# Performance work log

Measured on AMD Instinct MI355X. Metric: run time of the kernel, lower is better.

Reference implementation:

```python
import jax, jax.numpy as jnp
import numpy as np

HIDDEN = 3072
N_HEADS = 24
N_KV = 8
HEAD_DIM = HIDDEN // N_HEADS          # 128
ROT = int(HEAD_DIM * 0.75)            # 96 (partial rotary)
OP_SIZE = N_HEADS * HEAD_DIM + 2 * N_KV * HEAD_DIM  # 5120
LORA_R = 256
LORA_SCALE = 512.0 / LORA_R           # 2.0
ROPE_THETA = 10000.0
SCALE = HEAD_DIM ** -0.5


def setup_inputs() -> dict:
    key = jax.random.key(0)
    ks = jax.random.split(key, 8)
    B, S = 2, 2048
    hidden_states = jax.random.normal(ks[0], (B, S, HIDDEN), dtype=jnp.float32)
    position_ids = jnp.arange(B * S, dtype=jnp.int64 if jax.config.jax_enable_x64 else jnp.int32).reshape(B, S)
    w = lambda k, o, i: jax.random.normal(k, (o, i), dtype=jnp.float32) * (i ** -0.5)
    return {
        "hidden_states": hidden_states,
        "Wqkv": w(ks[1], OP_SIZE, HIDDEN),
        "Aqkv": w(ks[2], LORA_R, HIDDEN),
        "Bqkv": w(ks[3], OP_SIZE, LORA_R) * 0.01,
        "Wo": w(ks[4], HIDDEN, N_HEADS * HEAD_DIM),
        "Ao": w(ks[5], LORA_R, N_HEADS * HEAD_DIM),
        "Bo": w(ks[6], HIDDEN, LORA_R) * 0.01,
        "position_ids": position_ids,
    }


def _lora_linear(x, W, A, Bm):
    # base GEMM + low-rank LoRA update, scaling = alpha/r
    return x @ W.T + (x @ A.T) @ Bm.T * LORA_SCALE


def _rotate_half(x):
    h = x.shape[-1] // 2
    return jnp.concatenate((-x[..., h:], x[..., :h]), axis=-1)


def reference(hidden_states, Wqkv, Aqkv, Bqkv, Wo, Ao, Bo, position_ids):
    B, S, _ = hidden_states.shape
    qkv = _lora_linear(hidden_states, Wqkv, Aqkv, Bqkv)  # [B,S,5120]
    q_pos = N_HEADS * HEAD_DIM
    kv_pos = N_KV * HEAD_DIM
    q = qkv[..., :q_pos].reshape(B, S, N_HEADS, HEAD_DIM)
    k = qkv[..., q_pos:q_pos + kv_pos].reshape(B, S, N_KV, HEAD_DIM)
    v = qkv[..., q_pos + kv_pos:].reshape(B, S, N_KV, HEAD_DIM)

    # partial RoPE: cos/sin cache over rotary_ndims=96
    inv_freq = 1.0 / (ROPE_THETA ** (jnp.arange(0, ROT, 2, dtype=jnp.float32) / ROT))  # [48]
    freqs = position_ids.astype(jnp.float32)[..., None] * inv_freq  # [B,S,48]
    emb = jnp.concatenate((freqs, freqs), axis=-1)                   # [B,S,96]
    cos = jnp.cos(emb)[:, :, None, :]  # broadcast over head axis (bsnd)
    sin = jnp.sin(emb)[:, :, None, :]

    def rope(x):
        xr, xp = x[..., :ROT], x[..., ROT:]
        xr = xr * cos + _rotate_half(xr) * sin
        return jnp.concatenate((xr, xp), axis=-1)

    q = rope(q)
    k = rope(k)

    # GQA: repeat kv heads to match query heads
    groups = N_HEADS // N_KV
    k = jnp.repeat(k, groups, axis=2)
    v = jnp.repeat(v, groups, axis=2)

    scores = jnp.einsum('bqhd,bkhd->bhqk', q, k) * SCALE  # [B,H,S,S]
    causal = jnp.tril(jnp.ones((S, S), dtype=bool))
    scores = jnp.where(causal, scores, jnp.finfo(scores.dtype).min)
    probs = jax.nn.softmax(scores, axis=-1)
    attn = jnp.einsum('bhqk,bkhd->bqhd', probs, v).reshape(B, S, N_HEADS * HEAD_DIM)
    return _lora_linear(attn, Wo, Ao, Bo)
```

## Files before the change

### kernel.cpp

```cpp
#include <hip/hip_runtime.h>

typedef unsigned short u16;
typedef unsigned int   u32;

typedef __bf16 bf16_t;
typedef bf16_t bf16x8 __attribute__((ext_vector_type(8)));
typedef float  f32x4  __attribute__((ext_vector_type(4)));
typedef u16    u16x8  __attribute__((ext_vector_type(8)));

__device__ __forceinline__ float bf2f(u16 u) { return __uint_as_float(((u32)u) << 16); }
__device__ __forceinline__ u16 f2bf(float f) {
  u32 u = __float_as_uint(f);
  u32 r = u + 0x7fffu + ((u >> 16) & 1u);
  return (u16)(r >> 16);
}
__device__ __forceinline__ float fast_exp2(float x) { return __builtin_amdgcn_exp2f(x); }

__device__ __forceinline__ void gload_lds16(const u16* g, u16* l) {
  __builtin_amdgcn_global_load_lds(
      (const __attribute__((address_space(1))) void*)g,
      (__attribute__((address_space(3))) void*)l,
      16, 0, 0);
}

#define SBAR0() __builtin_amdgcn_sched_barrier(0)
#define HWBAR() __builtin_amdgcn_s_barrier()

__global__ void k_cast_str(const float* __restrict__ in, u16* __restrict__ out,
                           int C8, int L, int off, float scale) {
  const int r  = blockIdx.y;
  const int c8 = blockIdx.x * 128 + threadIdx.x;
  if (c8 >= C8) return;
  const f32x4* p = (const f32x4*)(in + (size_t)r * (C8 * 8) + c8 * 8);
  f32x4 a = p[0], b = p[1];
  u16x8 o;
  o[0] = f2bf(a[0] * scale); o[1] = f2bf(a[1] * scale);
  o[2] = f2bf(a[2] * scale); o[3] = f2bf(a[3] * scale);
  o[4] = f2bf(b[0] * scale); o[5] = f2bf(b[1] * scale);
  o[6] = f2bf(b[2] * scale); o[7] = f2bf(b[3] * scale);
  *(u16x8*)(out + (size_t)r * L + off + c8 * 8) = o;
}

__global__ void k_red4_cast(const float* __restrict__ t4, u16* __restrict__ out,
                            int C8, int L, int off, float scale, size_t plane) {
  const int r  = blockIdx.y;
  const int c8 = blockIdx.x * 64 + threadIdx.x;
  if (c8 >= C8) return;
  size_t base = (size_t)r * (C8 * 8) + c8 * 8;
  float s[8];
#pragma unroll
  for (int j = 0; j < 8; ++j) s[j] = 0.f;
#pragma unroll
  for (int p = 0; p < 4; ++p) {
    const f32x4* q = (const f32x4*)(t4 + p * plane + base);
    f32x4 a = q[0], b = q[1];
    s[0] += a[0]; s[1] += a[1]; s[2] += a[2]; s[3] += a[3];
    s[4] += b[0]; s[5] += b[1]; s[6] += b[2]; s[7] += b[3];
  }
  u16x8 o;
#pragma unroll
  for (int j = 0; j < 8; ++j) o[j] = f2bf(s[j] * scale);
  *(u16x8*)(out + (size_t)r * L + off + c8 * 8) = o;
}

__global__ __launch_bounds__(256) void k_gemm_bt_sk(
    const u16* __restrict__ A, const u16* __restrict__ B, float* __restrict__ C,
    int M, int N, int lda, int ldb, int kc) {
  __shared__ u16 As[64][64 + 8];
  __shared__ u16 Bs[64][64 + 8];
  const int tid   = threadIdx.x;
  const int lane  = tid & 63;
  const int w     = tid >> 6;
  const int wm    = (w >> 1) * 32;
  const int wn    = (w & 1) * 32;
  const int row16 = lane & 15;
  const int quad  = lane >> 4;
  const int m0 = blockIdx.y * 64;
  const int n0 = blockIdx.x * 64;
  const int ldr = tid >> 2;
  const int ldc = (tid & 3) * 16;
  const int z   = blockIdx.z;
  float* Cz = C + (size_t)z * M * N;
  const int kbeg = z * kc, kend = kbeg + kc;

  f32x4 acc[2][2] = {};

  for (int k0 = kbeg; k0 < kend; k0 += 64) {
    const u16* ga = A + (size_t)(m0 + ldr) * lda + (k0 + ldc);
    const u16* gb = B + (size_t)(n0 + ldr) * ldb + (k0 + ldc);
    u16x8 a0 = *(const u16x8*)ga;
    u16x8 a1 = *(const u16x8*)(ga + 8);
    u16x8 b0 = *(const u16x8*)gb;
    u16x8 b1 = *(const u16x8*)(gb + 8);
    __syncthreads();
    *(u16x8*)&As[ldr][ldc]     = a0;
    *(u16x8*)&As[ldr][ldc + 8] = a1;
    *(u16x8*)&Bs[ldr][ldc]     = b0;
    *(u16x8*)&Bs[ldr][ldc + 8] = b1;
    __syncthreads();
#pragma unroll
    for (int kk = 0; kk < 64; kk += 32) {
      bf16x8 af0 = *(const bf16x8*)&As[wm + row16][kk + quad * 8];
      bf16x8 af1 = *(const bf16x8*)&As[wm + 16 + row16][kk + quad * 8];
      bf16x8 bg0 = *(const bf16x8*)&Bs[wn + row16][kk + quad * 8];
      bf16x8 bg1 = *(const bf16x8*)&Bs[wn + 16 + row16][kk + quad * 8];
      acc[0][0] = __builtin_amdgcn_mfma_f32_16x16x32_bf16(af0, bg0, acc[0][0], 0, 0, 0);
      acc[0][1] = __builtin_amdgcn_mfma_f32_16x16x32_bf16(af0, bg1, acc[0][1], 0, 0, 0);
      acc[1][0] = __builtin_amdgcn_mfma_f32_16x16x32_bf16(af1, bg0, acc[1][0], 0, 0, 0);
      acc[1][1] = __builtin_amdgcn_mfma_f32_16x16x32_bf16(af1, bg1, acc[1][1], 0, 0, 0);
    }
  }
#pragma unroll
  for (int tm = 0; tm < 2; ++tm)
#pragma unroll
    for (int tn = 0; tn < 2; ++tn) {
      int gm = m0 + wm + tm * 16 + quad * 4;
      int gn = n0 + wn + tn * 16 + row16;
#pragma unroll
      for (int r = 0; r < 4; ++r)
        Cz[(size_t)(gm + r) * N + gn] = acc[tm][tn][r];
    }
}

__device__ __forceinline__ void stage_half(
    int H, int nt4,
    const u16* __restrict__ A, const u16* __restrict__ B, int K,
    int m0, int n0, u16* AsB, u16* BsB,
    int w, int rowin, int colsw) {
  if (H >= nt4) return;
  const int t = H >> 2, slot = H & 3;
  const int half = slot & 1;
  const u16* G = (slot < 2) ? A : B;
  const int r0 = (slot < 2) ? m0 : n0;
  u16* lds = ((slot < 2) ? AsB : BsB) + (t & 1) * 16384 + half * 8192;
  const int k0 = t * 64;
#pragma unroll
  for (int i = 0; i < 2; ++i) {
    const int chunk = w * 2 + i;
    const int row = half * 128 + chunk * 8 + rowin;
    gload_lds16(G + (size_t)(r0 + row) * K + k0 + colsw, lds + chunk * 512);
  }
}

__device__ __forceinline__ bf16x8 frag_ld(const u16* base, int row, int c16) {
  return *(const bf16x8*)(base + row * 64 + ((c16 ^ (row & 7)) << 3));
}

template <int RB>
__device__ __forceinline__ void gemm256_group(
    int k, int nt,
    const u16* __restrict__ A, const u16* __restrict__ B, int K,
    int m0, int n0, u16* AsB, u16* BsB,
    int wr, int wc, int row16, int quad, int w, int rowin, int colsw,
    f32x4 (&acc)[8][4]) {
  const u16* Ab = AsB + RB * 16384;
  const u16* Bb = BsB + RB * 16384;
  const int nt4 = nt * 4;
  bf16x8 a0[4][2], a1[4][2], b0[2][2], b1[2][2];

#pragma unroll
  for (int mf = 0; mf < 4; ++mf)
#pragma unroll
    for (int kk = 0; kk < 2; ++kk)
      a0[mf][kk] = frag_ld(Ab, wr * 128 + mf * 16 + row16, kk * 4 + quad);
#pragma unroll
  for (int nf = 0; nf < 2; ++nf)
#pragma unroll
    for (int kk = 0; kk < 2; ++kk)
      b0[nf][kk] = frag_ld(Bb, wc * 64 + nf * 16 + row16, kk * 4 + quad);
  stage_half(4 * k + 5, nt4, A, B, K, m0, n0, AsB, BsB, w, rowin, colsw);
  SBAR0(); HWBAR(); SBAR0();
  __builtin_amdgcn_s_setprio(1);
#pragma unroll
  for (int mf = 0; mf < 4; ++mf)
#pragma unroll
    for (int nf = 0; nf < 2; ++nf)
#pragma unroll
      for (int kk = 0; kk < 2; ++kk)
        acc[mf][nf] = __builtin_amdgcn_mfma_f32_16x16x32_bf16(a0[mf][kk], b0[nf][kk], acc[mf][nf], 0, 0, 0);
  __builtin_amdgcn_s_setprio(0);
  SBAR0(); HWBAR(); SBAR0();

#pragma unroll
  for (int nf = 0; nf < 2; ++nf)
#pragma unroll
    for (int kk = 0; kk < 2; ++kk)
      b1[nf][kk] = frag_ld(Bb, wc * 64 + 32 + nf * 16 + row16, kk * 4 + quad);
  stage_half(4 * k + 6, nt4, A, B, K, m0, n0, AsB, BsB, w, rowin, colsw);
  SBAR0(); HWBAR(); SBAR0();
  __builtin_amdgcn_s_setprio(1);
#pragma unroll
  for (int mf = 0; mf < 4; ++mf)
#pragma unroll
    for (int nf = 0; nf < 2; ++nf)
#pragma unroll
      for (int kk = 0; kk < 2; ++kk)
        acc[mf][2 + nf] = __builtin_amdgcn_mfma_f32_16x16x32_bf16(a0[mf][kk], b1[nf][kk], acc[mf][2 + nf], 0, 0, 0);
  __builtin_amdgcn_s_setprio(0);
  SBAR0(); HWBAR(); SBAR0();

#pragma unroll
  for (int mf = 0; mf < 4; ++mf)
#pragma unroll
    for (int kk = 0; kk < 2; ++kk)
      a1[mf][kk] = frag_ld(Ab, wr * 128 + 64 + mf * 16 + row16, kk * 4 + quad);
  stage_half(4 * k + 7, nt4, A, B, K, m0, n0, AsB, BsB, w, rowin, colsw);
  SBAR0(); HWBAR(); SBAR0();
  __builtin_amdgcn_s_setprio(1);
#pragma unroll
  for (int mf = 0; mf < 4; ++mf)
#pragma unroll
    for (int nf = 0; nf < 2; ++nf)
#pragma unroll
      for (int kk = 0; kk < 2; ++kk)
        acc[4 + mf][nf] = __builtin_amdgcn_mfma_f32_16x16x32_bf16(a1[mf][kk], b0[nf][kk], acc[4 + mf][nf], 0, 0, 0);
  __builtin_amdgcn_s_setprio(0);
  SBAR0(); HWBAR(); SBAR0();

  stage_half(4 * k + 8, nt4, A, B, K, m0, n0, AsB, BsB, w, rowin, colsw);
  SBAR0();
  if (k < nt - 2) { asm volatile("s_waitcnt vmcnt(2)" ::: "memory"); }
  else            { asm volatile("s_waitcnt vmcnt(0)" ::: "memory"); }
  HWBAR(); SBAR0();
  __builtin_amdgcn_s_setprio(1);
#pragma unroll
  for (int mf = 0; mf < 4; ++mf)
#pragma unroll
    for (int nf = 0; nf < 2; ++nf)
#pragma unroll
      for (int kk = 0; kk < 2; ++kk)
        acc[4 + mf][2 + nf] = __builtin_amdgcn_mfma_f32_16x16x32_bf16(a1[mf][kk], b1[nf][kk], acc[4 + mf][2 + nf], 0, 0, 0);
  __builtin_amdgcn_s_setprio(0);
  SBAR0(); HWBAR(); SBAR0();
}

__global__ __launch_bounds__(512, 2) void k_gemm256(
    const u16* __restrict__ A, const u16* __restrict__ B, float* __restrict__ C,
    int M, int N, int K) {
  __shared__ u16 As[2 * 16384];
  __shared__ u16 Bs[2 * 16384];

  const int tid   = threadIdx.x;
  const int lane  = tid & 63;
  const int w     = tid >> 6;
  const int wr    = w >> 2;
  const int wc    = w & 3;
  const int row16 = lane & 15;
  const int quad  = lane >> 4;
  const int rowin = lane >> 3;
  const int colsw = ((lane & 7) ^ (lane >> 3)) << 3;

  const int nwg = (int)gridDim.x;
  const int bid = (int)blockIdx.x;
  const int xcd = bid & 7, rest = bid >> 3;
  const int qq = nwg >> 3, rr = nwg & 7;
  const int wg = (xcd < rr ? xcd * (qq + 1) : rr * (qq + 1) + (xcd - rr) * qq) + rest;
  const int nbx = N >> 8;
  const int m0 = (wg / nbx) << 8;
  const int n0 = (wg % nbx) << 8;

  const int nt = K >> 6;
  f32x4 acc[8][4] = {};

#pragma unroll
  for (int H = 0; H < 5; ++H)
    stage_half(H, nt * 4, A, B, K, m0, n0, As, Bs, w, rowin, colsw);
  asm volatile("s_waitcnt vmcnt(2)" ::: "memory");
  HWBAR(); SBAR0();

  int k = 0;
  for (; k + 1 < nt; k += 2) {
    gemm256_group<0>(k,     nt, A, B, K, m0, n0, As, Bs, wr, wc, row16, quad, w, rowin, colsw, acc);
    gemm256_group<1>(k + 1, nt, A, B, K, m0, n0, As, Bs, wr, wc, row16, quad, w, rowin, colsw, acc);
  }
  if (k < nt)
    gemm256_group<0>(k, nt, A, B, K, m0, n0, As, Bs, wr, wc, row16, quad, w, rowin, colsw, acc);

#pragma unroll
  for (int mi = 0; mi < 8; ++mi) {
    const int gm = m0 + wr * 128 + mi * 16 + quad * 4;
#pragma unroll
    for (int nj = 0; nj < 4; ++nj) {
      const int gn = n0 + wc * 64 + nj * 16 + row16;
#pragma unroll
      for (int r = 0; r < 4; ++r)
        C[(size_t)(gm + r) * N + gn] = acc[mi][nj][r];
    }
  }
}

__global__ void k_rope_tab(const int* __restrict__ pos_ids, float* __restrict__ tab) {
  const int t = threadIdx.x;
  const int r = blockIdx.x * 4 + t / 48;
  const int j = t % 48;
  const float pos = (float)pos_ids[r];
  float invf = powf(10000.0f, -(float)j * (1.0f / 48.0f));
  float e = pos * invf;
  tab[(size_t)r * 96 + j]      = cosf(e);
  tab[(size_t)r * 96 + 48 + j] = sinf(e);
}

__global__ void k_rope_split(const float* __restrict__ qkv, const float* __restrict__ tab,
                             u16* __restrict__ qb, u16* __restrict__ kb) {
  const int r  = blockIdx.x;
  const int hh = blockIdx.y;
  const int d  = threadIdx.x;
  const float* src;
  if (hh < 24) src = qkv + (size_t)r * 5120 + hh * 128;
  else         src = qkv + (size_t)r * 5120 + 3072 + (hh - 24) * 128;
  float x = src[d];
  float outv;
  if (d >= 96) {
    outv = x;
  } else {
    int j = (d < 48) ? d : d - 48;
    float c  = tab[(size_t)r * 96 + j];
    float sn = tab[(size_t)r * 96 + 48 + j];
    if (d < 48) outv = x * c - src[d + 48] * sn;
    else        outv = x * c + src[d - 48] * sn;
  }
  u16 o = f2bf(outv);
  if (hh < 24) qb[((size_t)r * 24 + hh) * 128 + d] = o;
  else         kb[((size_t)r * 8 + (hh - 24)) * 128 + d] = o;
}

__global__ void k_vtrans(const float* __restrict__ qkv, u16* __restrict__ vtg) {
  const int d  = threadIdx.x;
  const int kg = blockIdx.x;
  const int bk = blockIdx.y;
  const int b = bk >> 3, kvh = bk & 7;
  const float* src = qkv + (size_t)(b * 2048 + kg * 8) * 5120 + 4096 + kvh * 128 + d;
  u16x8 pack;
#pragma unroll
  for (int t = 0; t < 8; ++t) pack[t] = f2bf(src[(size_t)t * 5120]);
  *(u16x8*)(vtg + ((size_t)bk * 128 + d) * 2048 + kg * 8) = pack;
}

__global__ __launch_bounds__(512) void k_attn_mfma(
    const u16* __restrict__ qb, const u16* __restrict__ kb, const u16* __restrict__ vtg,
    u16* __restrict__ attnw) {
  __shared__ u16 Ks[64 * 128];
  __shared__ u16 Vt[128 * 64];
  __shared__ u16 Ps[128 * 64];

  const int tid   = threadIdx.x;
  const int lane  = tid & 63;
  const int w     = tid >> 6;
  const int row16 = lane & 15;
  const int quad  = lane >> 4;
  const int qt  = (int)gridDim.x - 1 - (int)blockIdx.x;
  const int bh  = blockIdx.y;
  const int b   = bh / 24;
  const int h   = bh % 24;
  const int kvh = h / 3;
  const int q0  = qt * 128;
  const int qrow = q0 + w * 16 + row16;

  const u16* qbase = qb + (((size_t)(b * 2048 + qrow)) * 24 + h) * 128;
  bf16x8 qfrag[4];
#pragma unroll
  for (int kk = 0; kk < 4; ++kk) qfrag[kk] = *(const bf16x8*)(qbase + kk * 32 + quad * 8);

  const u16* kbbase = kb + ((size_t)(b * 2048) * 8 + kvh) * 128;
  const u16* vtbase = vtg + (size_t)(b * 8 + kvh) * 128 * 2048;

  f32x4 o[8] = {};
  float m_st = -INFINITY;
  float l_st = 0.f;
  const float C1 = 0.08838834764831845f * 1.4426950408889634f;

  const int ntile = 2 * qt + 2;

  u16x8 kr[2], vr[2];
#pragma unroll
  for (int i = 0; i < 2; ++i) {
    int c = tid + i * 512;
    kr[i] = *(const u16x8*)(kbbase + (size_t)(c >> 4) * 1024 + (c & 15) * 8);
  }
#pragma unroll
  for (int i = 0; i < 2; ++i) {
    int c = tid + i * 512;
    vr[i] = *(const u16x8*)(vtbase + (size_t)(c >> 3) * 2048 + (c & 7) * 8);
  }

  for (int t = 0; t < ntile; ++t) {
    const int kb0 = t * 64;
    __syncthreads();
#pragma unroll
    for (int i = 0; i < 2; ++i) {
      int c = tid + i * 512;
      int kk = c >> 4;
      int slot = (c & 15) ^ (kk & 7);
      *(u16x8*)&Ks[kk * 128 + slot * 8] = kr[i];
    }
#pragma unroll
    for (int i = 0; i < 2; ++i) {
      int c = tid + i * 512;
      int d = c >> 3;
      int slot = (c & 7) ^ (d & 7);
      *(u16x8*)&Vt[d * 64 + slot * 8] = vr[i];
    }
    __syncthreads();
    if (t + 1 < ntile) {
      const int nb0 = kb0 + 64;
#pragma unroll
      for (int i = 0; i < 2; ++i) {
        int c = tid + i * 512;
        kr[i] = *(const u16x8*)(kbbase + (size_t)(nb0 + (c >> 4)) * 1024 + (c & 15) * 8);
      }
#pragma unroll
      for (int i = 0; i < 2; ++i) {
        int c = tid + i * 512;
        vr[i] = *(const u16x8*)(vtbase + (size_t)(c >> 3) * 2048 + nb0 + (c & 7) * 8);
      }
    }

    f32x4 s[4] = {};
    __builtin_amdgcn_s_setprio(1);
#pragma unroll
    for (int kk = 0; kk < 4; ++kk) {
#pragma unroll
      for (int nt = 0; nt < 4; ++nt) {
        int krow = nt * 16 + row16;
        bf16x8 kfr = *(const bf16x8*)&Ks[krow * 128 + (((kk * 4 + quad) ^ (krow & 7)) << 3)];
        s[nt] = __builtin_amdgcn_mfma_f32_16x16x32_bf16(kfr, qfrag[kk], s[nt], 0, 0, 0);
      }
    }
    __builtin_amdgcn_s_setprio(0);

    if (t >= 2 * qt) {
#pragma unroll
      for (int nt = 0; nt < 4; ++nt) {
        int kbase = kb0 + nt * 16 + quad * 4;
#pragma unroll
        for (int r = 0; r < 4; ++r)
          if (kbase + r > qrow) s[nt][r] = -INFINITY;
      }
    }

    float mx = s[0][0];
#pragma unroll
    for (int nt = 0; nt < 4; ++nt)
#pragma unroll
      for (int r = 0; r < 4; ++r) mx = fmaxf(mx, s[nt][r]);
    mx = fmaxf(mx, __shfl_xor(mx, 16));
    mx = fmaxf(mx, __shfl_xor(mx, 32));
    float mnew = fmaxf(m_st, mx);
    float alpha = fast_exp2((m_st - mnew) * C1);
    m_st = mnew;
    float rs = 0.f;
#pragma unroll
    for (int nt = 0; nt < 4; ++nt)
#pragma unroll
      for (int r = 0; r < 4; ++r) {
        float p = fast_exp2((s[nt][r] - mnew) * C1);
        s[nt][r] = p;
        rs += p;
      }
    rs += __shfl_xor(rs, 16);
    rs += __shfl_xor(rs, 32);
    l_st = l_st * alpha + rs;
#pragma unroll
    for (int r = 0; r < 4; ++r) {
      float ar = __shfl(alpha, quad * 4 + r, 64);
#pragma unroll
      for (int dt = 0; dt < 8; ++dt) o[dt][r] *= ar;
    }

#pragma unroll
    for (int nt = 0; nt < 4; ++nt)
#pragma unroll
      for (int r = 0; r < 4; ++r) {
        int col = nt * 16 + quad * 4 + r;
        int slot = (col >> 3) ^ (row16 & 7);
        Ps[(w * 16 + row16) * 64 + slot * 8 + (col & 7)] = f2bf(s[nt][r]);
      }

    __builtin_amdgcn_s_setprio(1);
#pragma unroll
    for (int kk2 = 0; kk2 < 2; ++kk2) {
      bf16x8 pa = *(const bf16x8*)&Ps[(w * 16 + row16) * 64 + (((kk2 * 4 + quad) ^ (row16 & 7)) << 3)];
#pragma unroll
      for (int dt = 0; dt < 8; ++dt) {
        int vrow = dt * 16 + row16;
        bf16x8 vfr = *(const bf16x8*)&Vt[vrow * 64 + (((kk2 * 4 + quad) ^ (vrow & 7)) << 3)];
        o[dt] = __builtin_amdgcn_mfma_f32_16x16x32_bf16(pa, vfr, o[dt], 0, 0, 0);
      }
    }
    __builtin_amdgcn_s_setprio(0);
  }

#pragma unroll
  for (int r = 0; r < 4; ++r) {
    float lq = __shfl(l_st, quad * 4 + r, 64);
    float inv = 1.0f / lq;
    int row = q0 + w * 16 + quad * 4 + r;
    size_t obase = ((size_t)(b * 2048 + row)) * 3328 + (size_t)h * 128;
#pragma unroll
    for (int dt = 0; dt < 8; ++dt)
      attnw[obase + dt * 16 + row16] = f2bf(o[dt][r] * inv);
  }
}

#define OFF_XW    ((size_t)0)
#define OFF_WWQ   ((size_t)27262976)
#define OFF_AQKVB ((size_t)61341696)
#define OFF_WWO   ((size_t)62914560)
#define OFF_AOB   ((size_t)83361792)
#define OFF_QKV   ((size_t)84934656)
#define OFF_TA    ((size_t)168820736)
#define OFF_TA4   OFF_QKV
#define OFF_QB    OFF_XW
#define OFF_KB    OFF_WWQ
#define OFF_VTG   (OFF_WWQ + (size_t)8388608)
#define OFF_RTAB  (OFF_WWQ + (size_t)16777216)
#define OFF_ATTNW OFF_QKV
#define OFF_TO4   (OFF_QKV + (size_t)27262976)

extern "C" void kernel_launch(void* const* d_in, const int* in_sizes, int n_in,
                              void* d_out, int out_size, void* d_ws, size_t ws_size,
                              hipStream_t stream) {
  const float* x    = (const float*)d_in[0];
  const float* Wqkv = (const float*)d_in[1];
  const float* Aqkv = (const float*)d_in[2];
  const float* Bqkv = (const float*)d_in[3];
  const float* Wo   = (const float*)d_in[4];
  const float* Ao   = (const float*)d_in[5];
  const float* Bo   = (const float*)d_in[6];
  const int*   pos  = (const int*)d_in[7];
  float* out = (float*)d_out;
  char* ws = (char*)d_ws;

  u16* xw    = (u16*)(ws + OFF_XW);
  u16* wwq   = (u16*)(ws + OFF_WWQ);
  u16* aqkvb = (u16*)(ws + OFF_AQKVB);
  u16* wwo   = (u16*)(ws + OFF_WWO);
  u16* aob   = (u16*)(ws + OFF_AOB);
  float* qkv = (float*)(ws + OFF_QKV);
  float* tA  = (float*)(ws + OFF_TA);
  (void)tA;
  float* tA4 = (float*)(ws + OFF_TA4);
  u16* qb    = (u16*)(ws + OFF_QB);
  u16* kb    = (u16*)(ws + OFF_KB);
  u16* vtg   = (u16*)(ws + OFF_VTG);
  float* rtab = (float*)(ws + OFF_RTAB);
  u16* attnw = (u16*)(ws + OFF_ATTNW);
  float* tO4 = (float*)(ws + OFF_TO4);

  k_cast_str<<<dim3(3, 4096), 128, 0, stream>>>(x,    xw,  384, 3328, 0,    1.f);
  k_cast_str<<<dim3(3, 5120), 128, 0, stream>>>(Wqkv, wwq, 384, 3328, 0,    1.f);
  k_cast_str<<<dim3(1, 5120), 128, 0, stream>>>(Bqkv, wwq,  32, 3328, 3072, 1.f);
  k_cast_str<<<dim3(3, 256),  128, 0, stream>>>(Aqkv, aqkvb, 384, 3072, 0,  1.f);
  k_cast_str<<<dim3(3, 3072), 128, 0, stream>>>(Wo,   wwo, 384, 3328, 0,    1.f);
  k_cast_str<<<dim3(1, 3072), 128, 0, stream>>>(Bo,   wwo,  32, 3328, 3072, 1.f);
  k_cast_str<<<dim3(3, 256),  128, 0, stream>>>(Ao,   aob, 384, 3072, 0,    1.f);

  k_gemm_bt_sk<<<dim3(4, 64, 4), 256, 0, stream>>>(xw, aqkvb, tA4, 4096, 256, 3328, 3072, 768);
  k_red4_cast<<<dim3(1, 4096), 64, 0, stream>>>(tA4, xw, 32, 3328, 3072, 2.f, (size_t)4096 * 256);

  k_gemm256<<<dim3((5120 / 256) * (4096 / 256)), 512, 0, stream>>>(xw, wwq, qkv, 4096, 5120, 3328);

  k_rope_tab<<<dim3(1024), 192, 0, stream>>>(pos, rtab);
  k_rope_split<<<dim3(4096, 32), 128, 0, stream>>>(qkv, rtab, qb, kb);
  k_vtrans<<<dim3(256, 16), 128, 0, stream>>>(qkv, vtg);

  k_attn_mfma<<<dim3(16, 48), 512, 0, stream>>>(qb, kb, vtg, attnw);

  k_gemm_bt_sk<<<dim3(4, 64, 4), 256, 0, stream>>>(attnw, aob, tO4, 4096, 256, 3328, 3072, 768);
  k_red4_cast<<<dim3(1, 4096), 64, 0, stream>>>(tO4, attnw, 32, 3328, 3072, 2.f, (size_t)4096 * 256);

  k_gemm256<<<dim3((3072 / 256) * (4096 / 256)), 512, 0, stream>>>(attnw, wwo, out, 4096, 3072, 3328);
}
```

Before: 736.3 us.

## Restructure attention kernel with 32x32 MFMA, direct-to-LDS double buffering, and register P

Rewrites the flash-attention kernel to use 4 waves of 32 query rows with 32x32x16 MFMAs instead of 8 waves of 16 rows with 16x16x32. K/V tiles are loaded directly into double-buffered LDS via global_load_lds, which overlaps the next tile's load with compute and drops one barrier per tile. P is kept in registers using packed bf16 conversion and lane shuffles instead of a round trip through LDS. It also adds a lazy rescale that skips updating the running max and the O rescale when the max grows only a little, and stages the output through LDS for vectorized stores. The costs are higher register pressure and the extra bounded-error logic in the softmax.

```diff
diff --git a/kernel.cpp b/kernel.cpp
--- a/kernel.cpp
+++ b/kernel.cpp
@@ -6,7 +6,9 @@
 typedef __bf16 bf16_t;
 typedef bf16_t bf16x8 __attribute__((ext_vector_type(8)));
 typedef float  f32x4  __attribute__((ext_vector_type(4)));
+typedef float  f32x16 __attribute__((ext_vector_type(16)));
 typedef u16    u16x8  __attribute__((ext_vector_type(8)));
+typedef u32    u32x4  __attribute__((ext_vector_type(4)));
 
 __device__ __forceinline__ float bf2f(u16 u) { return __uint_as_float(((u32)u) << 16); }
 __device__ __forceinline__ u16 f2bf(float f) {
@@ -336,169 +338,180 @@
   *(u16x8*)(vtg + ((size_t)bk * 128 + d) * 2048 + kg * 8) = pack;
 }
 
-__global__ __launch_bounds__(512) void k_attn_mfma(
+__global__ __launch_bounds__(256) void k_attn_mfma(
     const u16* __restrict__ qb, const u16* __restrict__ kb, const u16* __restrict__ vtg,
     u16* __restrict__ attnw) {
-  __shared__ u16 Ks[64 * 128];
-  __shared__ u16 Vt[128 * 64];
-  __shared__ u16 Ps[128 * 64];
-
-  const int tid   = threadIdx.x;
-  const int lane  = tid & 63;
-  const int w     = tid >> 6;
-  const int row16 = lane & 15;
-  const int quad  = lane >> 4;
-  const int qt  = (int)gridDim.x - 1 - (int)blockIdx.x;
-  const int bh  = blockIdx.y;
-  const int b   = bh / 24;
-  const int h   = bh % 24;
-  const int kvh = h / 3;
-  const int q0  = qt * 128;
-  const int qrow = q0 + w * 16 + row16;
-
-  const u16* qbase = qb + (((size_t)(b * 2048 + qrow)) * 24 + h) * 128;
-  bf16x8 qfrag[4];
-#pragma unroll
-  for (int kk = 0; kk < 4; ++kk) qfrag[kk] = *(const bf16x8*)(qbase + kk * 32 + quad * 8);
+  __shared__ u16 KsA[8192], VtA[8192], KsB[8192], VtB[8192];
+
+  const int tid  = threadIdx.x;
+  const int lane = tid & 63;
+  const int w    = tid >> 6;
+  const int l31  = lane & 31;
+  const int hi   = lane >> 5;
+  const int r7   = lane & 7;
+  const int qt   = (int)gridDim.x - 1 - (int)blockIdx.x;
+  const int bh   = blockIdx.y;
+  const int b    = bh / 24;
+  const int h    = bh % 24;
+  const int kvh  = h / 3;
+  const int q0   = qt * 128;
+  const int qrow = q0 + w * 32 + l31;
+
+  const u16* qrb = qb + (((size_t)(b * 2048 + qrow)) * 24 + h) * 128;
+  bf16x8 qf[8];
+#pragma unroll
+  for (int kk = 0; kk < 8; ++kk) qf[kk] = *(const bf16x8*)(qrb + kk * 16 + hi * 8);
 
   const u16* kbbase = kb + ((size_t)(b * 2048) * 8 + kvh) * 128;
   const u16* vtbase = vtg + (size_t)(b * 8 + kvh) * 128 * 2048;
 
-  f32x4 o[8] = {};
-  float m_st = -INFINITY;
-  float l_st = 0.f;
+  f32x16 o32[4] = {};
+  float m_st = -INFINITY, l_st = 0.f;
   const float C1 = 0.08838834764831845f * 1.4426950408889634f;
-
   const int ntile = 2 * qt + 2;
 
-  u16x8 kr[2], vr[2];
-#pragma unroll
-  for (int i = 0; i < 2; ++i) {
-    int c = tid + i * 512;
-    kr[i] = *(const u16x8*)(kbbase + (size_t)(c >> 4) * 1024 + (c & 15) * 8);
-  }
-#pragma unroll
-  for (int i = 0; i < 2; ++i) {
-    int c = tid + i * 512;
-    vr[i] = *(const u16x8*)(vtbase + (size_t)(c >> 3) * 2048 + (c & 7) * 8);
-  }
+#define STAGE(Kd, Vd, KB0)                                                          \
+  {                                                                                 \
+    _Pragma("unroll")                                                               \
+    for (int i = 0; i < 4; ++i) {                                                   \
+      const int c = w * 4 + i;                                                      \
+      const int rowk = 4 * c + (lane >> 4);                                         \
+      gload_lds16(kbbase + (size_t)((KB0) + rowk) * 1024 +                          \
+                      (((lane & 15) ^ (rowk & 7)) << 3),                            \
+                  (Kd) + c * 512);                                                  \
+      const int rowv = 8 * c + (lane >> 3);                                         \
+      gload_lds16(vtbase + (size_t)rowv * 2048 + (KB0) +                            \
+                      (((lane & 7) ^ (rowv & 7)) << 3),                             \
+                  (Vd) + c * 512);                                                  \
+    }                                                                               \
+  }
+
+  STAGE(KsA, VtA, 0);
+  __syncthreads();
 
   for (int t = 0; t < ntile; ++t) {
     const int kb0 = t * 64;
+    const u16* Kc = (t & 1) ? KsB : KsA;
+    const u16* Vc = (t & 1) ? VtB : VtA;
+    if (t + 1 < ntile) {
+      u16* Kn = (t & 1) ? KsA : KsB;
+      u16* Vn = (t & 1) ? VtA : VtB;
+      STAGE(Kn, Vn, kb0 + 64);
+    }
+
+    f32x16 s[2] = {};
+    __builtin_amdgcn_s_setprio(1);
+#pragma unroll
+    for (int kk = 0; kk < 8; ++kk) {
+#pragma unroll
+      for (int kt = 0; kt < 2; ++kt) {
+        const int row = kt * 32 + l31;
+        bf16x8 kf = *(const bf16x8*)&Kc[row * 128 + (((2 * kk + hi) ^ r7) << 3)];
+        s[kt] = __builtin_amdgcn_mfma_f32_32x32x16_bf16(kf, qf[kk], s[kt], 0, 0, 0);
+      }
+    }
+    __builtin_amdgcn_s_setprio(0);
+
+    if (kb0 >= q0) {
+#pragma unroll
+      for (int kt = 0; kt < 2; ++kt)
+#pragma unroll
+        for (int r = 0; r < 16; ++r) {
+          const int key = kb0 + 32 * kt + (r & 3) + 8 * (r >> 2) + 4 * hi;
+          if (key > qrow) s[kt][r] = -INFINITY;
+        }
+    }
+
+    float tm[16];
+#pragma unroll
+    for (int r = 0; r < 16; ++r) tm[r] = fmaxf(s[0][r], s[1][r]);
+#pragma unroll
+    for (int st = 8; st >= 1; st >>= 1)
+#pragma unroll
+      for (int r = 0; r < 8; ++r)
+        if (r < st) tm[r] = fmaxf(tm[r], tm[r + st]);
+    float mx = fmaxf(tm[0], __shfl_xor(tm[0], 32));
+
+    const bool skip = __all((mx - m_st) * C1 <= 8.0f);
+    if (!skip) {
+      const float mnew = fmaxf(m_st, mx);
+      const float alpha = fast_exp2((m_st - mnew) * C1);
+      l_st *= alpha;
+#pragma unroll
+      for (int dt = 0; dt < 4; ++dt)
+#pragma unroll
+        for (int r = 0; r < 16; ++r) o32[dt][r] *= alpha;
+      m_st = mnew;
+    }
+    const float mc = m_st * C1;
+    float ts[16];
+#pragma unroll
+    for (int r = 0; r < 16; ++r) {
+      float p0 = fast_exp2(__builtin_fmaf(s[0][r], C1, -mc));
+      float p1 = fast_exp2(__builtin_fmaf(s[1][r], C1, -mc));
+      s[0][r] = p0; s[1][r] = p1;
+      ts[r] = p0 + p1;
+    }
+#pragma unroll
+    for (int st = 8; st >= 1; st >>= 1)
+#pragma unroll
+      for (int r = 0; r < 8; ++r)
+        if (r < st) ts[r] += ts[r + st];
+    l_st += ts[0] + __shfl_xor(ts[0], 32);
+
+    bf16x8 pb[4];
+#pragma unroll
+    for (int kt = 0; kt < 2; ++kt) {
+      u32 pk[8];
+#pragma unroll
+      for (int i = 0; i < 8; ++i)
+        asm("v_cvt_pk_bf16_f32 %0, %1, %2"
+            : "=v"(pk[i]) : "v"(s[kt][2 * i]), "v"(s[kt][2 * i + 1]));
+      u32 e0 = __shfl_xor(hi ? pk[0] : pk[2], 32);
+      u32 e1 = __shfl_xor(hi ? pk[1] : pk[3], 32);
+      u32 e2 = __shfl_xor(hi ? pk[4] : pk[6], 32);
+      u32 e3 = __shfl_xor(hi ? pk[5] : pk[7], 32);
+      u32x4 w0, w1;
+      w0[0] = hi ? e0 : pk[0]; w0[1] = hi ? e1 : pk[1];
+      w0[2] = hi ? pk[2] : e0; w0[3] = hi ? pk[3] : e1;
+      w1[0] = hi ? e2 : pk[4]; w1[1] = hi ? e3 : pk[5];
+      w1[2] = hi ? pk[6] : e2; w1[3] = hi ? pk[7] : e3;
+      pb[2 * kt]     = __builtin_bit_cast(bf16x8, w0);
+      pb[2 * kt + 1] = __builtin_bit_cast(bf16x8, w1);
+    }
+
+    __builtin_amdgcn_s_setprio(1);
+#pragma unroll
+    for (int ks = 0; ks < 4; ++ks) {
+#pragma unroll
+      for (int dt = 0; dt < 4; ++dt) {
+        const int vrow = dt * 32 + l31;
+        bf16x8 vf = *(const bf16x8*)&Vc[vrow * 64 + (((2 * ks + hi) ^ r7) << 3)];
+        o32[dt] = __builtin_amdgcn_mfma_f32_32x32x16_bf16(vf, pb[ks], o32[dt], 0, 0, 0);
+      }
+    }
+    __builtin_amdgcn_s_setprio(0);
+
     __syncthreads();
-#pragma unroll
-    for (int i = 0; i < 2; ++i) {
-      int c = tid + i * 512;
-      int kk = c >> 4;
-      int slot = (c & 15) ^ (kk & 7);
-      *(u16x8*)&Ks[kk * 128 + slot * 8] = kr[i];
-    }
-#pragma unroll
-    for (int i = 0; i < 2; ++i) {
-      int c = tid + i * 512;
-      int d = c >> 3;
-      int slot = (c & 7) ^ (d & 7);
-      *(u16x8*)&Vt[d * 64 + slot * 8] = vr[i];
-    }
-    __syncthreads();
-    if (t + 1 < ntile) {
-      const int nb0 = kb0 + 64;
-#pragma unroll
-      for (int i = 0; i < 2; ++i) {
-        int c = tid + i * 512;
-        kr[i] = *(const u16x8*)(kbbase + (size_t)(nb0 + (c >> 4)) * 1024 + (c & 15) * 8);
-      }
-#pragma unroll
-      for (int i = 0; i < 2; ++i) {
-        int c = tid + i * 512;
-        vr[i] = *(const u16x8*)(vtbase + (size_t)(c >> 3) * 2048 + nb0 + (c & 7) * 8);
-      }
-    }
-
-    f32x4 s[4] = {};
-    __builtin_amdgcn_s_setprio(1);
-#pragma unroll
-    for (int kk = 0; kk < 4; ++kk) {
-#pragma unroll
-      for (int nt = 0; nt < 4; ++nt) {
-        int krow = nt * 16 + row16;
-        bf16x8 kfr = *(const bf16x8*)&Ks[krow * 128 + (((kk * 4 + quad) ^ (krow & 7)) << 3)];
-        s[nt] = __builtin_amdgcn_mfma_f32_16x16x32_bf16(kfr, qfrag[kk], s[nt], 0, 0, 0);
-      }
-    }
-    __builtin_amdgcn_s_setprio(0);
-
-    if (t >= 2 * qt) {
-#pragma unroll
-      for (int nt = 0; nt < 4; ++nt) {
-        int kbase = kb0 + nt * 16 + quad * 4;
-#pragma unroll
-        for (int r = 0; r < 4; ++r)
-          if (kbase + r > qrow) s[nt][r] = -INFINITY;
-      }
-    }
-
-    float mx = s[0][0];
-#pragma unroll
-    for (int nt = 0; nt < 4; ++nt)
-#pragma unroll
-      for (int r = 0; r < 4; ++r) mx = fmaxf(mx, s[nt][r]);
-    mx = fmaxf(mx, __shfl_xor(mx, 16));
-    mx = fmaxf(mx, __shfl_xor(mx, 32));
-    float mnew = fmaxf(m_st, mx);
-    float alpha = fast_exp2((m_st - mnew) * C1);
-    m_st = mnew;
-    float rs = 0.f;
-#pragma unroll
-    for (int nt = 0; nt < 4; ++nt)
-#pragma unroll
-      for (int r = 0; r < 4; ++r) {
-        float p = fast_exp2((s[nt][r] - mnew) * C1);
-        s[nt][r] = p;
-        rs += p;
-      }
-    rs += __shfl_xor(rs, 16);
-    rs += __shfl_xor(rs, 32);
-    l_st = l_st * alpha + rs;
-#pragma unroll
-    for (int r = 0; r < 4; ++r) {
-      float ar = __shfl(alpha, quad * 4 + r, 64);
-#pragma unroll
-      for (int dt = 0; dt < 8; ++dt) o[dt][r] *= ar;
-    }
-
-#pragma unroll
-    for (int nt = 0; nt < 4; ++nt)
-#pragma unroll
-      for (int r = 0; r < 4; ++r) {
-        int col = nt * 16 + quad * 4 + r;
-        int slot = (col >> 3) ^ (row16 & 7);
-        Ps[(w * 16 + row16) * 64 + slot * 8 + (col & 7)] = f2bf(s[nt][r]);
-      }
-
-    __builtin_amdgcn_s_setprio(1);
-#pragma unroll
-    for (int kk2 = 0; kk2 < 2; ++kk2) {
-      bf16x8 pa = *(const bf16x8*)&Ps[(w * 16 + row16) * 64 + (((kk2 * 4 + quad) ^ (row16 & 7)) << 3)];
-#pragma unroll
-      for (int dt = 0; dt < 8; ++dt) {
-        int vrow = dt * 16 + row16;
-        bf16x8 vfr = *(const bf16x8*)&Vt[vrow * 64 + (((kk2 * 4 + quad) ^ (vrow & 7)) << 3)];
-        o[dt] = __builtin_amdgcn_mfma_f32_16x16x32_bf16(pa, vfr, o[dt], 0, 0, 0);
-      }
-    }
-    __builtin_amdgcn_s_setprio(0);
-  }
-
-#pragma unroll
-  for (int r = 0; r < 4; ++r) {
-    float lq = __shfl(l_st, quad * 4 + r, 64);
-    float inv = 1.0f / lq;
-    int row = q0 + w * 16 + quad * 4 + r;
-    size_t obase = ((size_t)(b * 2048 + row)) * 3328 + (size_t)h * 128;
-#pragma unroll
-    for (int dt = 0; dt < 8; ++dt)
-      attnw[obase + dt * 16 + row16] = f2bf(o[dt][r] * inv);
+  }
+
+  const float inv = 1.0f / l_st;
+  u16* scr = ((w < 2) ? KsA : VtA) + (w & 1) * 4096;
+#pragma unroll
+  for (int dt = 0; dt < 4; ++dt)
+#pragma unroll
+    for (int r = 0; r < 16; ++r) {
+      const int d = 32 * dt + (r & 3) + 8 * (r >> 2) + 4 * hi;
+      const int slot = (d >> 3) ^ (l31 & 7);
+      scr[l31 * 128 + slot * 8 + (d & 7)] = f2bf(o32[dt][r] * inv);
+    }
+  const int q32r = lane >> 1, part = lane & 1;
+  const size_t grow = ((size_t)(b * 2048 + q0 + w * 32 + q32r)) * 3328 + (size_t)h * 128;
+#pragma unroll
+  for (int c = 0; c < 8; ++c) {
+    const int d0 = part * 64 + c * 8;
+    const int s2 = (d0 >> 3) ^ (q32r & 7);
+    *(u16x8*)(attnw + grow + d0) = *(const u16x8*)&scr[q32r * 128 + s2 * 8];
   }
 }
 
@@ -537,8 +550,6 @@
   u16* wwo   = (u16*)(ws + OFF_WWO);
   u16* aob   = (u16*)(ws + OFF_AOB);
   float* qkv = (float*)(ws + OFF_QKV);
-  float* tA  = (float*)(ws + OFF_TA);
-  (void)tA;
   float* tA4 = (float*)(ws + OFF_TA4);
   u16* qb    = (u16*)(ws + OFF_QB);
   u16* kb    = (u16*)(ws + OFF_KB);
@@ -564,7 +575,7 @@
   k_rope_split<<<dim3(4096, 32), 128, 0, stream>>>(qkv, rtab, qb, kb);
   k_vtrans<<<dim3(256, 16), 128, 0, stream>>>(qkv, vtg);
 
-  k_attn_mfma<<<dim3(16, 48), 512, 0, stream>>>(qb, kb, vtg, attnw);
+  k_attn_mfma<<<dim3(16, 48), 256, 0, stream>>>(qb, kb, vtg, attnw);
 
   k_gemm_bt_sk<<<dim3(4, 64, 4), 256, 0, stream>>>(attnw, aob, tO4, 4096, 256, 3328, 3072, 768);
   k_red4_cast<<<dim3(1, 4096), 64, 0, stream>>>(tO4, attnw, 32, 3328, 3072, 2.f, (size_t)4096 * 256);
```

Result: no change. 734.5 us (-0.2%).
